# Kernel optimization log

Measured on AMD Instinct MI355X. Metric: run time of the kernel, lower is better.

## Reference

```python
import jax, jax.numpy as jnp
import numpy as np

B, R = 2, 4096
N_COARSE, N_IMP = 48, 48
RAY_START, RAY_END = 0.1, 1.0
BOX_WARP = 2.0
C_PLANE, H_PLANE = 32, 256
HIDDEN = 64

_P = np.array([[[1, 0, 0], [0, 1, 0], [0, 0, 1]],
               [[1, 0, 0], [0, 0, 1], [0, 1, 0]],
               [[0, 0, 1], [1, 0, 0], [0, 1, 0]]], np.float32)
INV_PLANES = jnp.asarray(np.linalg.inv(_P))  # [3,3,3]


def _gs_one(f, g):
    # f: [C,H,W]; g: [M,2] in [-1,1]; bilinear, zeros padding, align_corners=False
    C, H, W = f.shape
    x = (g[:, 0] + 1.0) * (W / 2) - 0.5
    y = (g[:, 1] + 1.0) * (H / 2) - 0.5
    x0 = jnp.floor(x); y0 = jnp.floor(y)
    xi0 = x0.astype(jnp.int32); yi0 = y0.astype(jnp.int32)
    fx = x - x0; fy = y - y0
    out = jnp.zeros((C, g.shape[0]), f.dtype)
    for dx in (0, 1):
        for dy in (0, 1):
            xi = xi0 + dx; yi = yi0 + dy
            w = (fx if dx else 1.0 - fx) * (fy if dy else 1.0 - fy)
            valid = (xi >= 0) & (xi < W) & (yi >= 0) & (yi < H)
            val = f[:, jnp.clip(yi, 0, H - 1), jnp.clip(xi, 0, W - 1)]  # [C,M]
            out = out + jnp.where(valid, w, 0.0)[None, :] * val
    return out

grid_sample_2d = jax.vmap(_gs_one)


def sample_from_planes(plane_feats, coords):
    # plane_feats [B,3,C,H,W], coords [B,M,3] -> [B,M,C] (mean over planes)
    b, nP, C, H, W = plane_feats.shape
    c = (2.0 / BOX_WARP) * coords
    proj = jnp.einsum('bmk,pkj->bpmj', c, INV_PLANES)[..., :2]  # [B,3,M,2]
    out = grid_sample_2d(plane_feats.reshape(b * nP, C, H, W), proj.reshape(b * nP, -1, 2))
    return out.reshape(b, nP, C, -1).mean(1).transpose(0, 2, 1)


def decoder(tex_f, shp_f, W1, b1, W2, b2):
    x = jnp.concatenate([tex_f, shp_f], -1)          # [B,M,2C]
    h = jax.nn.softplus(x @ W1 + b1)
    o = h @ W2 + b2
    sigma = o[..., :1]
    rgb = jax.nn.sigmoid(o[..., 1:]) * (1 + 2 * 0.001) - 0.001
    return rgb, sigma


def ray_march(colors, densities, depths):
    # MipRayMarcher2: midpoint compositing, softplus(density-1), alpha compositing
    deltas = depths[:, :, 1:] - depths[:, :, :-1]
    c_mid = (colors[:, :, :-1] + colors[:, :, 1:]) * 0.5
    d_mid = (densities[:, :, :-1] + densities[:, :, 1:]) * 0.5
    z_mid = (depths[:, :, :-1] + depths[:, :, 1:]) * 0.5
    dens = jax.nn.softplus(d_mid - 1.0)
    alpha = 1.0 - jnp.exp(-dens * deltas)
    shifted = jnp.concatenate([jnp.ones_like(alpha[:, :, :1]), 1.0 - alpha + 1e-10], 2)
    weights = alpha * jnp.cumprod(shifted, 2)[:, :, :-1]
    rgb = (weights * c_mid).sum(2)
    wt = weights.sum(2)
    depth = jnp.nan_to_num((weights * z_mid).sum(2) / wt, posinf=0.0)
    depth = jnp.clip(depth, depths.min(), depths.max())
    return rgb * 2.0 - 1.0, depth, weights


def sample_pdf(bins, weights, u):
    # bins [P,Nb], weights [P,Nw], u [P,Ni] -> inverse-CDF samples [P,Ni]
    pdf = weights / jnp.sum(weights, -1, keepdims=True)
    cdf = jnp.cumsum(pdf, -1)
    cdf = jnp.concatenate([jnp.zeros_like(cdf[:, :1]), cdf], -1)
    inds = jax.vmap(lambda c, uu: jnp.searchsorted(c, uu, side='right'))(cdf, u)
    below = jnp.maximum(inds - 1, 0)
    above = jnp.minimum(inds, weights.shape[-1])
    cdf0 = jnp.take_along_axis(cdf, below, 1)
    cdf1 = jnp.take_along_axis(cdf, above, 1)
    b0 = jnp.take_along_axis(bins, below, 1)
    b1v = jnp.take_along_axis(bins, above, 1)
    denom = cdf1 - cdf0
    denom = jnp.where(denom < 1e-5, 1.0, denom)
    t = (u - cdf0) / denom
    return b0 + t * (b1v - b0)


def sample_importance(depths, weights, u):
    b, r, n1, _ = weights.shape  # n1 = N_COARSE - 1
    w = weights.reshape(b * r, n1)
    # max_pool1d(k=2, s=1, pad=1) then avg_pool1d(k=2, s=1), then +0.01 (weights >= 0)
    wp = jnp.concatenate([jnp.zeros_like(w[:, :1]), w, jnp.zeros_like(w[:, :1])], 1)
    w = jnp.maximum(wp[:, :-1], wp[:, 1:])
    w = 0.5 * (w[:, :-1] + w[:, 1:]) + 0.01
    z = depths.reshape(b * r, -1)
    z_mid = 0.5 * (z[:, :-1] + z[:, 1:])
    fine = sample_pdf(z_mid, w[:, 1:-1], u.reshape(b * r, -1))
    return jax.lax.stop_gradient(fine.reshape(b, r, -1, 1))  # .detach() in torch


def run_model(planes_tex, planes_shp, coords, W1, b1, W2, b2):
    tex_f = sample_from_planes(planes_tex, coords)
    shp_f = sample_from_planes(planes_shp, coords)
    return decoder(tex_f, shp_f, W1, b1, W2, b2)


def reference(planes_tex, planes_shp, ray_origins, ray_directions, W1, b1, W2, b2, strat_noise, imp_u):
    dirs = ray_directions / jnp.linalg.norm(ray_directions, axis=-1, keepdims=True)
    b, r, _ = ray_origins.shape
    delta = (RAY_END - RAY_START) / (N_COARSE - 1)
    base = RAY_START + delta * jnp.arange(N_COARSE, dtype=jnp.float32)
    depths_c = base.reshape(1, 1, N_COARSE, 1) + strat_noise * delta  # [B,R,Nc,1]
    coords_c = (ray_origins[:, :, None] + depths_c * dirs[:, :, None]).reshape(b, -1, 3)
    rgb_c, sig_c = run_model(planes_tex, planes_shp, coords_c, W1, b1, W2, b2)
    rgb_c = rgb_c.reshape(b, r, N_COARSE, 3)
    sig_c = sig_c.reshape(b, r, N_COARSE, 1)
    _, _, weights = ray_march(rgb_c, sig_c, depths_c)
    depths_f = sample_importance(depths_c, weights, imp_u)  # [B,R,Ni,1]
    coords_f = (ray_origins[:, :, None] + depths_f * dirs[:, :, None]).reshape(b, -1, 3)
    rgb_f, sig_f = run_model(planes_tex, planes_shp, coords_f, W1, b1, W2, b2)
    rgb_f = rgb_f.reshape(b, r, N_IMP, 3)
    sig_f = sig_f.reshape(b, r, N_IMP, 1)
    all_d = jnp.concatenate([depths_c, depths_f], 2)
    all_c = jnp.concatenate([rgb_c, rgb_f], 2)
    all_s = jnp.concatenate([sig_c, sig_f], 2)
    idx = jnp.argsort(all_d, axis=2)
    all_d = jnp.take_along_axis(all_d, idx, 2)
    all_c = jnp.take_along_axis(all_c, jnp.broadcast_to(idx, all_c.shape), 2)
    all_s = jnp.take_along_axis(all_s, idx, 2)
    rgb_final, depth_final, w_all = ray_march(all_c, all_s, all_d)
    return rgb_final, depth_final, w_all.sum(2)


def setup_inputs() -> dict:
    key = jax.random.key(0)
    ks = jax.random.split(key, 8)
    return {
        'planes_tex': jax.random.normal(ks[0], (B, 3, C_PLANE, H_PLANE, H_PLANE), jnp.float32),
        'planes_shp': jax.random.normal(ks[1], (B, 3, C_PLANE, H_PLANE, H_PLANE), jnp.float32),
        'ray_origins': 0.3 * jax.random.normal(ks[2], (B, R, 3), jnp.float32),
        'ray_directions': jax.random.normal(ks[3], (B, R, 3), jnp.float32),
        'W1': jax.random.normal(ks[4], (2 * C_PLANE, HIDDEN), jnp.float32) / np.sqrt(2 * C_PLANE),
        'b1': jnp.zeros((HIDDEN,), jnp.float32),
        'W2': jax.random.normal(ks[5], (HIDDEN, 4), jnp.float32) / np.sqrt(HIDDEN),
        'b2': jnp.zeros((4,), jnp.float32),
        'strat_noise': jax.random.uniform(ks[6], (B, R, N_COARSE, 1), jnp.float32),
        'imp_u': jax.random.uniform(ks[7], (B, R, N_IMP), jnp.float32),
    }
```

## Files before the change

### kernel.cpp

```cpp
#include <hip/hip_runtime.h>
#include <hip/hip_fp16.h>
#include <math.h>

#define NRAY 8192
#define NC_  48
#define NI_  48
#define HPL  256
#define HID  64
#define NPTS (NRAY * NC_)
#define BPTS 64

typedef __attribute__((ext_vector_type(8))) _Float16 half8;
typedef __attribute__((ext_vector_type(4))) float f32x4;

__device__ __forceinline__ float softplusf(float x) {
    return fmaxf(x, 0.0f) + __logf(1.0f + __expf(-fabsf(x)));
}
__device__ __forceinline__ float sigmoidf(float x) {
    return 1.0f / (1.0f + __expf(-x));
}

#define TR_BLOCKS 3072
__global__ __launch_bounds__(256) void setup_kernel(
    const float* __restrict__ tex, const float* __restrict__ shp,
    __half* __restrict__ planes_cl,
    const float* __restrict__ W1, const float* __restrict__ b1, const float* __restrict__ W2,
    __half* __restrict__ w1f, float* __restrict__ w2f, float* __restrict__ b1f,
    float* __restrict__ part_mn, float* __restrict__ part_mx,
    const float* __restrict__ noise,
    const float* __restrict__ origins, const float* __restrict__ dirs,
    float* __restrict__ rayod)
{
    __shared__ __half t2[256][34];
    __shared__ float smn[4], smx[4];
    int b = blockIdx.x;
    int tid = threadIdx.x;
    if (b < TR_BLOCKS) {
        int p = b >> 8;
        int y = b & 255;
        const float* in = (p < 6) ? tex : shp;
        int pp    = (p < 6) ? p : p - 6;
        int choff = (p < 6) ? 0 : 32;
        const float* base = in + ((size_t)(pp * 32) * 256 + y) * 256;
        int lane6 = tid & 63;
        int cb    = (tid >> 6) * 8;
        int x0    = lane6 * 4;
#pragma unroll
        for (int i = 0; i < 8; ++i) {
            float4 v = *(const float4*)(base + (size_t)(cb + i) * 65536 + x0);
            t2[x0 + 0][cb + i] = __float2half(v.x);
            t2[x0 + 1][cb + i] = __float2half(v.y);
            t2[x0 + 2][cb + i] = __float2half(v.z);
            t2[x0 + 3][cb + i] = __float2half(v.w);
        }
        __syncthreads();
        __half* outRow = planes_cl + ((size_t)(pp * 256 + y) * 256) * 64 + choff;
#pragma unroll
        for (int it = 0; it < 4; ++it) {
            int idx = it * 256 + tid;
            int x = idx >> 2, c8 = (idx & 3) * 8;
            *(uint4*)(outRow + (size_t)x * 64 + c8) = *(const uint4*)&t2[x][c8];
        }
    } else if (b == TR_BLOCKS) {
        int l = tid;
        if (l < 64) {
            int g = l >> 4, c = l & 15;
#pragma unroll
            for (int t = 0; t < 4; ++t) {
#pragma unroll
                for (int kb = 0; kb < 2; ++kb)
#pragma unroll
                    for (int j = 0; j < 8; ++j)
                        w1f[((t * 2 + kb) * 64 + l) * 8 + j] =
                            __float2half(W1[(kb * 32 + g * 8 + j) * HID + t * 16 + c]);
#pragma unroll
                for (int o = 0; o < 4; ++o) w2f[(t * 64 + l) * 4 + o] = W2[(t * 16 + c) * 4 + o];
                b1f[t * 64 + l] = b1[t * 16 + c];
            }
        }
    } else if (b < TR_BLOCKS + 17) {
        int bl = b - TR_BLOCKS - 1;
        int gtid = bl * 256 + tid;
        float mn = INFINITY, mx = -INFINITY;
        for (int r = gtid; r < NRAY; r += 4096) {
            mn = fminf(mn, noise[r * NC_]);
            mx = fmaxf(mx, noise[r * NC_ + NC_ - 1]);
        }
#pragma unroll
        for (int mask = 1; mask <= 32; mask <<= 1) {
            mn = fminf(mn, __shfl_xor(mn, mask, 64));
            mx = fmaxf(mx, __shfl_xor(mx, mask, 64));
        }
        int wv = tid >> 6;
        if ((tid & 63) == 0) { smn[wv] = mn; smx[wv] = mx; }
        __syncthreads();
        if (tid == 0) {
#pragma unroll
            for (int i = 1; i < 4; ++i) { mn = fminf(mn, smn[i]); mx = fmaxf(mx, smx[i]); }
            const float delta = (1.0f - 0.1f) / (NC_ - 1);
            part_mn[bl] = 0.1f + mn * delta;
            part_mx[bl] = 0.1f + delta * 47.0f + mx * delta;
        }
    } else {
        int ray = (b - TR_BLOCKS - 17) * 256 + tid;
        float ox = origins[ray * 3 + 0], oy = origins[ray * 3 + 1], oz = origins[ray * 3 + 2];
        float dx = dirs[ray * 3 + 0], dy = dirs[ray * 3 + 1], dz = dirs[ray * 3 + 2];
        float invn = 1.0f / sqrtf(dx * dx + dy * dy + dz * dz);
        dx *= invn; dy *= invn; dz *= invn;
        float4 A4 = make_float4(ox, oy, oz, dx);
        float4 B4 = make_float4(dy, dz, 0.0f, 0.0f);
        *(float4*)(rayod + (size_t)ray * 8)     = A4;
        *(float4*)(rayod + (size_t)ray * 8 + 4) = B4;
    }
}

template<bool FINE>
__global__ __launch_bounds__(256, 8) void fused_sample_mlp(
    const __half* __restrict__ planes,
    const float* __restrict__ rayod,
    const float* __restrict__ noise,
    const float* __restrict__ impu,
    const float* __restrict__ depths_c,
    const float4* __restrict__ rgbs_c_in,
    float* __restrict__ depths_out,
    const __half* __restrict__ w1f, const float* __restrict__ w2f,
    const float* __restrict__ b1f, const float* __restrict__ b2,
    float4* __restrict__ outRGBS)
{
    __shared__ __half lds_x[BPTS][72];
    __shared__ int s_tap[BPTS][12][2];
    __shared__ float s_cdf[2][48];
    __shared__ float s_zm[2][48];

    int tid = threadIdx.x;
    int r0 = (blockIdx.x * BPTS) / NC_;

    if constexpr (FINE) {
        int wv = tid >> 6, lane = tid & 63;
        int r1 = (blockIdx.x * BPTS + BPTS - 1) / NC_;
        if (wv <= r1 - r0) {
            int ray = r0 + wv;
            float d = 0.f, sg = 0.f;
            if (lane < NC_) {
                d  = depths_c[ray * NC_ + lane];
                sg = rgbs_c_in[ray * NC_ + lane].w;
            }
            float dn = __shfl_down(d, 1, 64);
            float sn = __shfl_down(sg, 1, 64);
            bool iv = (lane < NC_ - 1);
            float zm = 0.5f * (d + dn);
            float alpha = 0.f, f = 1.0f;
            if (iv) {
                float dens = softplusf(0.5f * (sg + sn) - 1.0f);
                alpha = 1.0f - __expf(-dens * (dn - d));
                f = 1.0f - alpha + 1e-10f;
            }
            float x = f;
#pragma unroll
            for (int s = 1; s < 64; s <<= 1) {
                float t = __shfl_up(x, s, 64);
                if (lane >= s) x *= t;
            }
            float excl = __shfl_up(x, 1, 64);
            if (lane == 0) excl = 1.0f;
            float w = alpha * excl;
            float wprev = __shfl_up(w, 1, 64);
            float wmax;
            if (lane == 0) wmax = w;
            else if (lane == NC_ - 1) wmax = wprev;
            else wmax = fmaxf(wprev, w);
            float wmaxn = __shfl_down(wmax, 1, 64);
            float wb = 0.5f * (wmax + wmaxn) + 0.01f;
            float v = (lane >= 1 && lane <= 45) ? wb : 0.0f;
            float ssum = v;
#pragma unroll
            for (int mask = 1; mask <= 32; mask <<= 1) ssum += __shfl_xor(ssum, mask, 64);
            float pdf = v / ssum;
            float cum = pdf;
#pragma unroll
            for (int st = 1; st < 64; st <<= 1) {
                float t = __shfl_up(cum, st, 64);
                if (lane >= st) cum += t;
            }
            if (lane <= 45) s_cdf[wv][lane] = (lane == 0) ? 0.0f : cum;
            if (iv) s_zm[wv][lane] = zm;
        }
        __syncthreads();
    }

    if (tid < 192) {
        int p  = tid & 63;
        int pp = tid >> 6;
        int point = blockIdx.x * BPTS + p;
        int ray = point / NC_;
        int bIdx = ray >> 12;

        float t;
        if constexpr (!FINE) {
            int s = point - ray * NC_;
            const float delta = (1.0f - 0.1f) / (NC_ - 1);
            t = 0.1f + delta * (float)s + noise[point] * delta;
        } else {
            int ridx = ray - r0;
            float u = impu[point];
            const float* cdf = s_cdf[ridx];
            const float* zmp = s_zm[ridx];
            int lo = 0, hi = 46;
            while (lo < hi) { int mid = (lo + hi) >> 1; if (cdf[mid] > u) hi = mid; else lo = mid + 1; }
            int below = max(lo - 1, 0);
            int above = min(lo, 45);
            float c0 = cdf[below], c1 = cdf[above];
            float b0 = zmp[below], b1v = zmp[above];
            float den = c1 - c0; if (den < 1e-5f) den = 1.0f;
            t = b0 + (u - c0) / den * (b1v - b0);
        }
        if (pp == 0) depths_out[point] = t;

        const float4 A4 = *(const float4*)(rayod + (size_t)ray * 8);
        const float4 B4 = *(const float4*)(rayod + (size_t)ray * 8 + 4);
        float px = A4.x + t * A4.w;
        float py = A4.y + t * B4.x;
        float pz = A4.z + t * B4.y;

        float U = (pp == 2) ? pz : px;
        float V = (pp == 0) ? py : ((pp == 1) ? pz : px);
        const float inv3 = 1.0f / 3.0f;

        float gx = (U + 1.0f) * 128.0f - 0.5f;
        float gy = (V + 1.0f) * 128.0f - 0.5f;
        float fgx = floorf(gx), fgy = floorf(gy);
        int x0 = (int)fgx, y0 = (int)fgy;
        float fx = gx - fgx, fy = gy - fgy;
#pragma unroll
        for (int k = 0; k < 4; ++k) {
            int dxk = k & 1, dyk = k >> 1;
            int xi = x0 + dxk, yi = y0 + dyk;
            float w = (dxk ? fx : 1.0f - fx) * (dyk ? fy : 1.0f - fy);
            bool valid = (xi >= 0) && (xi < HPL) && (yi >= 0) && (yi < HPL);
            int xc = min(max(xi, 0), HPL - 1);
            int yc = min(max(yi, 0), HPL - 1);
            int p3 = bIdx * 3 + pp;
            __half2 hw2 = __half2half2(__float2half(valid ? w * inv3 : 0.0f));
            s_tap[p][pp * 4 + k][0] = (((p3 * HPL) + yc) * HPL + xc) * 64;
            s_tap[p][pp * 4 + k][1] = *(const int*)&hw2;
        }
    }
    __syncthreads();

#pragma unroll 1
    for (int round = 0; round < 2; ++round) {
        int p = (tid >> 3) + round * 32;
        int sub = tid & 7;
        int off[12];
        int wb[12];
#pragma unroll
        for (int kk = 0; kk < 12; ++kk) {
            off[kk] = s_tap[p][kk][0];
            wb[kk]  = s_tap[p][kk][1];
        }
        __half2 acc2[4];
#pragma unroll
        for (int i = 0; i < 4; ++i) acc2[i] = __half2half2(__float2half(0.0f));
#pragma unroll
        for (int kk = 0; kk < 12; ++kk) {
            __half2 w2 = *(const __half2*)&wb[kk];
            float4 v = *(const float4*)(planes + off[kk] + sub * 8);
            union { float4 f; __half2 h[4]; } u;
            u.f = v;
#pragma unroll
            for (int i = 0; i < 4; ++i) acc2[i] = __hfma2(u.h[i], w2, acc2[i]);
        }
        *(uint4*)&lds_x[p][sub * 8] = *(const uint4*)&acc2[0];
    }
    __syncthreads();

    int lane = tid & 63, wave = tid >> 6;
    {
        int g = lane >> 4, c = lane & 15;
        int mrow = wave * 16 + c;
        half8 a0 = *(const half8*)(&lds_x[mrow][g * 8]);
        half8 a1 = *(const half8*)(&lds_x[mrow][32 + g * 8]);

        float o[4][4];
#pragma unroll
        for (int r = 0; r < 4; ++r)
#pragma unroll
            for (int q = 0; q < 4; ++q) o[r][q] = 0.0f;

#pragma unroll
        for (int t = 0; t < 4; ++t) {
            half8 bf0 = *(const half8*)(w1f + ((size_t)((t * 2 + 0) * 64 + lane)) * 8);
            half8 bf1 = *(const half8*)(w1f + ((size_t)((t * 2 + 1) * 64 + lane)) * 8);
            f32x4 z = {0.f, 0.f, 0.f, 0.f};
            z = __builtin_amdgcn_mfma_f32_16x16x32_f16(a0, bf0, z, 0, 0, 0);
            z = __builtin_amdgcn_mfma_f32_16x16x32_f16(a1, bf1, z, 0, 0, 0);
            float  b1s = b1f[t * 64 + lane];
            float4 w2  = *(const float4*)(w2f + (size_t)(t * 64 + lane) * 4);
#pragma unroll
            for (int r = 0; r < 4; ++r) {
                float sp = softplusf(z[r] + b1s);
                o[r][0] = fmaf(sp, w2.x, o[r][0]);
                o[r][1] = fmaf(sp, w2.y, o[r][1]);
                o[r][2] = fmaf(sp, w2.z, o[r][2]);
                o[r][3] = fmaf(sp, w2.w, o[r][3]);
            }
        }
#pragma unroll
        for (int mask = 1; mask <= 8; mask <<= 1)
#pragma unroll
            for (int r = 0; r < 4; ++r)
#pragma unroll
                for (int q = 0; q < 4; ++q) o[r][q] += __shfl_xor(o[r][q], mask, 64);

        if (c == 0) {
#pragma unroll
            for (int r = 0; r < 4; ++r) {
                int pt = blockIdx.x * BPTS + wave * 16 + g * 4 + r;
                float sig = o[r][0] + b2[0];
                float rr = sigmoidf(o[r][1] + b2[1]) * 1.002f - 0.001f;
                float gg = sigmoidf(o[r][2] + b2[2]) * 1.002f - 0.001f;
                float bb = sigmoidf(o[r][3] + b2[3]) * 1.002f - 0.001f;
                outRGBS[pt] = make_float4(rr, gg, bb, sig);
            }
        }
    }
}

#define FM_WAVES 4
__global__ __launch_bounds__(256) void final_march(
    const float* __restrict__ depths_c, const float4* __restrict__ rgbs_c,
    const float* __restrict__ depths_f, const float4* __restrict__ rgbs_f,
    const float* __restrict__ part_mn, const float* __restrict__ part_mx,
    float* __restrict__ out)
{
    __shared__ float s_dc[FM_WAVES][NC_];
    __shared__ float s_df[FM_WAVES][NI_];
    __shared__ float s_md[FM_WAVES][96];
    __shared__ float s_ms[FM_WAVES][96];
    __shared__ float s_mr[FM_WAVES][96];
    __shared__ float s_mg[FM_WAVES][96];
    __shared__ float s_mb[FM_WAVES][96];

    int wave = threadIdx.x >> 6, lane = threadIdx.x & 63;
    int ray = blockIdx.x * FM_WAVES + wave;
    float* dcp = s_dc[wave];
    float* dfp = s_df[wave];
    float* mdp = s_md[wave];
    float* msp = s_ms[wave];
    float* mrp = s_mr[wave];
    float* mgp = s_mg[wave];
    float* mbp = s_mb[wave];

    float dcv = 0.f, dfv = 0.f;
    float4 c4 = make_float4(0, 0, 0, 0), f4 = make_float4(0, 0, 0, 0);
    if (lane < NC_) {
        dcv = depths_c[ray * NC_ + lane];
        dfv = depths_f[ray * NI_ + lane];
        dcp[lane] = dcv;
        dfp[lane] = dfv;
        c4 = rgbs_c[ray * NC_ + lane];
        f4 = rgbs_f[ray * NI_ + lane];
    }
    __syncthreads();

    if (lane < NC_) {
        int cntC = 0, rankF = 0, cntCle = 0;
#pragma unroll
        for (int j = 0; j < NC_; ++j) {
            float dfj = dfp[j];
            float dcj = dcp[j];
            cntC   += (dfj < dcv) ? 1 : 0;
            rankF  += ((dfj < dfv) || (dfj == dfv && j < lane)) ? 1 : 0;
            cntCle += (dcj <= dfv) ? 1 : 0;
        }
        int posC = lane + cntC;
        int posF = rankF + cntCle;
        mdp[posC] = dcv; msp[posC] = c4.w; mrp[posC] = c4.x; mgp[posC] = c4.y; mbp[posC] = c4.z;
        mdp[posF] = dfv; msp[posF] = f4.w; mrp[posF] = f4.x; mgp[posF] = f4.y; mbp[posF] = f4.z;
    }
    __syncthreads();

    int k0 = 2 * lane;
    int i0 = min(k0, 95), i1 = min(k0 + 1, 95), i2 = min(k0 + 2, 95);
    float d0 = mdp[i0], d1 = mdp[i1], d2 = mdp[i2];
    float sg0 = msp[i0], sg1 = msp[i1], sg2 = msp[i2];
    float r0 = mrp[i0], r1 = mrp[i1], r2 = mrp[i2];
    float g0 = mgp[i0], g1 = mgp[i1], g2 = mgp[i2];
    float bb0 = mbp[i0], bb1 = mbp[i1], bb2 = mbp[i2];

    bool v0 = (k0 < 95), v1 = (k0 + 1 < 95);
    float a0 = 0.f, a1 = 0.f, f0 = 1.f, f1 = 1.f;
    if (v0) {
        float dens = softplusf(0.5f * (sg0 + sg1) - 1.0f);
        a0 = 1.0f - __expf(-dens * (d1 - d0));
        f0 = 1.0f - a0 + 1e-10f;
    }
    if (v1) {
        float dens = softplusf(0.5f * (sg1 + sg2) - 1.0f);
        a1 = 1.0f - __expf(-dens * (d2 - d1));
        f1 = 1.0f - a1 + 1e-10f;
    }

    float pl = f0 * f1;
    float x = pl;
#pragma unroll
    for (int d = 1; d < 64; d <<= 1) {
        float t = __shfl_up(x, d, 64);
        if (lane >= d) x *= t;
    }
    float excl = __shfl_up(x, 1, 64);
    if (lane == 0) excl = 1.0f;
    float w0 = a0 * excl;
    float w1 = a1 * excl * f0;

    float accR = w0 * 0.5f * (r0 + r1) + w1 * 0.5f * (r1 + r2);
    float accG = w0 * 0.5f * (g0 + g1) + w1 * 0.5f * (g1 + g2);
    float accB = w0 * 0.5f * (bb0 + bb1) + w1 * 0.5f * (bb1 + bb2);
    float accD = w0 * 0.5f * (d0 + d1) + w1 * 0.5f * (d1 + d2);
    float accW = w0 + w1;
#pragma unroll
    for (int mask = 1; mask <= 32; mask <<= 1) {
        accR += __shfl_xor(accR, mask, 64);
        accG += __shfl_xor(accG, mask, 64);
        accB += __shfl_xor(accB, mask, 64);
        accD += __shfl_xor(accD, mask, 64);
        accW += __shfl_xor(accW, mask, 64);
    }

    float pmn = (lane < 16) ? part_mn[lane] : INFINITY;
    float pmx = (lane < 16) ? part_mx[lane] : -INFINITY;
#pragma unroll
    for (int mask = 1; mask <= 32; mask <<= 1) {
        pmn = fminf(pmn, __shfl_xor(pmn, mask, 64));
        pmx = fmaxf(pmx, __shfl_xor(pmx, mask, 64));
    }

    if (lane == 0) {
        float q = accD / accW;
        if (!isfinite(q)) q = 0.0f;
        q = fminf(fmaxf(q, pmn), pmx);
        out[ray * 3 + 0] = accR * 2.0f - 1.0f;
        out[ray * 3 + 1] = accG * 2.0f - 1.0f;
        out[ray * 3 + 2] = accB * 2.0f - 1.0f;
        out[3 * NRAY + ray] = q;
        out[4 * NRAY + ray] = accW;
    }
}

extern "C" void kernel_launch(void* const* d_in, const int* in_sizes, int n_in,
                              void* d_out, int out_size, void* d_ws, size_t ws_size,
                              hipStream_t stream)
{
    const float* planes_tex = (const float*)d_in[0];
    const float* planes_shp = (const float*)d_in[1];
    const float* origins    = (const float*)d_in[2];
    const float* raydirs    = (const float*)d_in[3];
    const float* W1 = (const float*)d_in[4];
    const float* b1 = (const float*)d_in[5];
    const float* W2 = (const float*)d_in[6];
    const float* b2 = (const float*)d_in[7];
    const float* noise = (const float*)d_in[8];
    const float* impu  = (const float*)d_in[9];
    float* out = (float*)d_out;

    char* ws = (char*)d_ws;
    __half*         planes_cl = (__half*)ws;
    __half*         w1f       = (__half*)(ws + 50331648);
    float*          w2f       = (float*)(ws + 50339840);
    float*          b1f       = (float*)(ws + 50343936);
    float*          part_mn   = (float*)(ws + 50344960);
    float*          part_mx   = (float*)(ws + 50345024);
    float*  depths_c = (float*)(ws + 50345216);
    float*  depths_f = (float*)(ws + 51918080);
    float4* rgbs_c   = (float4*)(ws + 53490944);
    float4* rgbs_f   = (float4*)(ws + 59782400);
    float*  rayod    = (float*)(ws + 66073856);

    setup_kernel<<<dim3(TR_BLOCKS + 1 + 16 + 32), dim3(256), 0, stream>>>(
        planes_tex, planes_shp, planes_cl, W1, b1, W2, w1f, w2f, b1f, part_mn, part_mx,
        noise, origins, raydirs, rayod);

    fused_sample_mlp<false><<<dim3(NPTS / BPTS), dim3(256), 0, stream>>>(
        planes_cl, rayod, noise, nullptr, nullptr, nullptr,
        depths_c, w1f, w2f, b1f, b2, rgbs_c);

    fused_sample_mlp<true><<<dim3(NPTS / BPTS), dim3(256), 0, stream>>>(
        planes_cl, rayod, nullptr, impu, depths_c, rgbs_c,
        depths_f, w1f, w2f, b1f, b2, rgbs_f);

    final_march<<<dim3(NRAY / FM_WAVES), dim3(256), 0, stream>>>(
        depths_c, rgbs_c, depths_f, rgbs_f, part_mn, part_mx, out);
}
```

Baseline: 271.5 us.

## Double points per block, add compact sigma buffer, repad transpose LDS

Each sampling/MLP block now handles 128 points instead of 64, with loops over sample tasks, gather rounds and MFMA halves, and the occupancy hint is lowered to match. The coarse pass also writes sigma to a separate float array, so the fine pass's CDF construction reads 4 bytes per sample instead of a float4. The setup transpose's LDS row padding changes from 34 to 40 halves to alter its bank pattern. The larger tile amortizes per-block CDF and setup work, but raises register and LDS pressure and may cut resident waves.

```diff
diff --git a/kernel.cpp b/kernel.cpp
--- a/kernel.cpp
+++ b/kernel.cpp
@@ -8,7 +8,7 @@
 #define HPL  256
 #define HID  64
 #define NPTS (NRAY * NC_)
-#define BPTS 64
+#define BPTS 128
 
 typedef __attribute__((ext_vector_type(8))) _Float16 half8;
 typedef __attribute__((ext_vector_type(4))) float f32x4;
@@ -31,7 +31,7 @@
     const float* __restrict__ origins, const float* __restrict__ dirs,
     float* __restrict__ rayod)
 {
-    __shared__ __half t2[256][34];
+    __shared__ __half t2[256][40];
     __shared__ float smn[4], smx[4];
     int b = blockIdx.x;
     int tid = threadIdx.x;
@@ -115,22 +115,23 @@
 }
 
 template<bool FINE>
-__global__ __launch_bounds__(256, 8) void fused_sample_mlp(
+__global__ __launch_bounds__(256, 5) void fused_sample_mlp(
     const __half* __restrict__ planes,
     const float* __restrict__ rayod,
     const float* __restrict__ noise,
     const float* __restrict__ impu,
     const float* __restrict__ depths_c,
-    const float4* __restrict__ rgbs_c_in,
+    const float* __restrict__ sigc,
     float* __restrict__ depths_out,
     const __half* __restrict__ w1f, const float* __restrict__ w2f,
     const float* __restrict__ b1f, const float* __restrict__ b2,
-    float4* __restrict__ outRGBS)
+    float4* __restrict__ outRGBS,
+    float* __restrict__ sig_out)
 {
     __shared__ __half lds_x[BPTS][72];
     __shared__ int s_tap[BPTS][12][2];
-    __shared__ float s_cdf[2][48];
-    __shared__ float s_zm[2][48];
+    __shared__ float s_cdf[4][48];
+    __shared__ float s_zm[4][48];
 
     int tid = threadIdx.x;
     int r0 = (blockIdx.x * BPTS) / NC_;
@@ -143,7 +144,7 @@
             float d = 0.f, sg = 0.f;
             if (lane < NC_) {
                 d  = depths_c[ray * NC_ + lane];
-                sg = rgbs_c_in[ray * NC_ + lane].w;
+                sg = sigc[ray * NC_ + lane];
             }
             float dn = __shfl_down(d, 1, 64);
             float sn = __shfl_down(sg, 1, 64);
@@ -188,9 +189,10 @@
         __syncthreads();
     }
 
-    if (tid < 192) {
-        int p  = tid & 63;
-        int pp = tid >> 6;
+#pragma unroll 1
+    for (int task = tid; task < 3 * BPTS; task += 256) {
+        int p  = task & (BPTS - 1);
+        int pp = task >> 7;
         int point = blockIdx.x * BPTS + p;
         int ray = point / NC_;
         int bIdx = ray >> 12;
@@ -241,43 +243,46 @@
             int yc = min(max(yi, 0), HPL - 1);
             int p3 = bIdx * 3 + pp;
             __half2 hw2 = __half2half2(__float2half(valid ? w * inv3 : 0.0f));
-            s_tap[p][pp * 4 + k][0] = (((p3 * HPL) + yc) * HPL + xc) * 64;
+            s_tap[p][pp * 4 + k][0] = (((p3 * HPL) + yc) * HPL + xc) * 128;
             s_tap[p][pp * 4 + k][1] = *(const int*)&hw2;
         }
     }
     __syncthreads();
 
+    {
+        const char* pbase = (const char*)planes + (tid & 7) * 16;
 #pragma unroll 1
-    for (int round = 0; round < 2; ++round) {
-        int p = (tid >> 3) + round * 32;
-        int sub = tid & 7;
-        int off[12];
-        int wb[12];
-#pragma unroll
-        for (int kk = 0; kk < 12; ++kk) {
-            off[kk] = s_tap[p][kk][0];
-            wb[kk]  = s_tap[p][kk][1];
-        }
-        __half2 acc2[4];
-#pragma unroll
-        for (int i = 0; i < 4; ++i) acc2[i] = __half2half2(__float2half(0.0f));
-#pragma unroll
-        for (int kk = 0; kk < 12; ++kk) {
-            __half2 w2 = *(const __half2*)&wb[kk];
-            float4 v = *(const float4*)(planes + off[kk] + sub * 8);
-            union { float4 f; __half2 h[4]; } u;
-            u.f = v;
-#pragma unroll
-            for (int i = 0; i < 4; ++i) acc2[i] = __hfma2(u.h[i], w2, acc2[i]);
-        }
-        *(uint4*)&lds_x[p][sub * 8] = *(const uint4*)&acc2[0];
+        for (int round = 0; round < 4; ++round) {
+            int p = (tid >> 3) + round * 32;
+            int off[12];
+            int wb[12];
+#pragma unroll
+            for (int kk = 0; kk < 12; ++kk) {
+                off[kk] = s_tap[p][kk][0];
+                wb[kk]  = s_tap[p][kk][1];
+            }
+            __half2 acc2[4];
+#pragma unroll
+            for (int i = 0; i < 4; ++i) acc2[i] = __half2half2(__float2half(0.0f));
+#pragma unroll
+            for (int kk = 0; kk < 12; ++kk) {
+                __half2 w2 = *(const __half2*)&wb[kk];
+                float4 v = *(const float4*)(pbase + off[kk]);
+                union { float4 f; __half2 h[4]; } u;
+                u.f = v;
+#pragma unroll
+                for (int i = 0; i < 4; ++i) acc2[i] = __hfma2(u.h[i], w2, acc2[i]);
+            }
+            *(uint4*)&lds_x[p][(tid & 7) * 8] = *(const uint4*)&acc2[0];
+        }
     }
     __syncthreads();
 
     int lane = tid & 63, wave = tid >> 6;
-    {
-        int g = lane >> 4, c = lane & 15;
-        int mrow = wave * 16 + c;
+    int g = lane >> 4, c = lane & 15;
+#pragma unroll 1
+    for (int half = 0; half < 2; ++half) {
+        int mrow = wave * 32 + half * 16 + c;
         half8 a0 = *(const half8*)(&lds_x[mrow][g * 8]);
         half8 a1 = *(const half8*)(&lds_x[mrow][32 + g * 8]);
 
@@ -315,12 +320,13 @@
         if (c == 0) {
 #pragma unroll
             for (int r = 0; r < 4; ++r) {
-                int pt = blockIdx.x * BPTS + wave * 16 + g * 4 + r;
+                int pt = blockIdx.x * BPTS + wave * 32 + half * 16 + g * 4 + r;
                 float sig = o[r][0] + b2[0];
                 float rr = sigmoidf(o[r][1] + b2[1]) * 1.002f - 0.001f;
                 float gg = sigmoidf(o[r][2] + b2[2]) * 1.002f - 0.001f;
                 float bb = sigmoidf(o[r][3] + b2[3]) * 1.002f - 0.001f;
                 outRGBS[pt] = make_float4(rr, gg, bb, sig);
+                if constexpr (!FINE) sig_out[pt] = sig;
             }
         }
     }
@@ -475,6 +481,7 @@
     float4* rgbs_c   = (float4*)(ws + 53490944);
     float4* rgbs_f   = (float4*)(ws + 59782400);
     float*  rayod    = (float*)(ws + 66073856);
+    float*  sigc     = (float*)(ws + 66336000);
 
     setup_kernel<<<dim3(TR_BLOCKS + 1 + 16 + 32), dim3(256), 0, stream>>>(
         planes_tex, planes_shp, planes_cl, W1, b1, W2, w1f, w2f, b1f, part_mn, part_mx,
@@ -482,11 +489,11 @@
 
     fused_sample_mlp<false><<<dim3(NPTS / BPTS), dim3(256), 0, stream>>>(
         planes_cl, rayod, noise, nullptr, nullptr, nullptr,
-        depths_c, w1f, w2f, b1f, b2, rgbs_c);
+        depths_c, w1f, w2f, b1f, b2, rgbs_c, sigc);
 
     fused_sample_mlp<true><<<dim3(NPTS / BPTS), dim3(256), 0, stream>>>(
-        planes_cl, rayod, nullptr, impu, depths_c, rgbs_c,
-        depths_f, w1f, w2f, b1f, b2, rgbs_f);
+        planes_cl, rayod, nullptr, impu, depths_c, sigc,
+        depths_f, w1f, w2f, b1f, b2, rgbs_f, nullptr);
 
     final_march<<<dim3(NRAY / FM_WAVES), dim3(256), 0, stream>>>(
         depths_c, rgbs_c, depths_f, rgbs_f, part_mn, part_mx, out);
```

Result: slower. 281.4 us (+3.6%).
